# Kernel optimization log

Measured on AMD Instinct MI355X. Metric: run time of the kernel, lower is better.

## Reference

```python
import jax, jax.numpy as jnp
import numpy as np

G, DIN, DOUT, R = 8, 1024, 1024, 16
N = 8192
SCALE = 32.0 / 16.0  # alpha / r


def grouped_linear(x, W, mask):
    """Grouped linear: out[n] = x[n] @ W[g[n]].
    x: [N, din], W: [G, din, dout], mask: [N, G] one-hot (float).
    Computed as all-group matmul + select; the fused grouped-GEMM is the
    kernel opportunity this reference baselines."""
    y_all = jnp.einsum('ni,gio->gno', x, W)      # [G, N, dout]
    return jnp.einsum('gno,ng->no', y_all, mask)  # [N, dout]


def setup_inputs() -> dict:
    key = jax.random.key(0)
    k1, k2, k3, k4, k5 = jax.random.split(key, 5)
    x = jax.random.normal(k1, (N, DIN), dtype=jnp.float32)
    x_groups = jnp.sort(jax.random.randint(k2, (N,), 0, G, dtype=jnp.int64))
    W_base = jax.random.normal(k3, (G, DIN, DOUT), dtype=jnp.float32) * 0.02
    W_A = jax.random.normal(k4, (G, DIN, R), dtype=jnp.float32) * 0.02
    # original inits lora_B to zero; use small random values so the LoRA path
    # contributes nonzero signal for correctness testing
    W_B = jax.random.normal(k5, (G, R, DOUT), dtype=jnp.float32) * 0.02
    return {"x": x, "x_groups": x_groups, "W_base": W_base, "W_A": W_A, "W_B": W_B}


def reference(x, x_groups, W_base, W_A, W_B):
    mask = (x_groups[:, None] == jnp.arange(G)).astype(x.dtype)  # [N, G] one-hot
    base = grouped_linear(x, W_base, mask)            # base GroupedLinear
    a = grouped_linear(x, W_A, mask)                  # lora_A (dropout p=0 -> identity)
    adapt = grouped_linear(a, W_B, mask)              # lora_B
    return base + SCALE * adapt
```

## Files before the change

### kernel.cpp

```cpp
#include <hip/hip_runtime.h>
#include <stdint.h>

#define N_TOK 8192
#define DIN   1024
#define DOUT  1024
#define NG    8
#define LSCALE 2.0f

typedef __attribute__((ext_vector_type(4))) float  float4v;
typedef __attribute__((ext_vector_type(8))) short  short8;
typedef short8  frag_ab;
typedef float4v frag_cd;

__device__ __forceinline__ short f2bf(float f) {
    union { float f; uint32_t u; } v; v.f = f;
    uint32_t r = v.u + 0x7fffu + ((v.u >> 16) & 1u);
    return (short)(r >> 16);
}

__device__ __forceinline__ void load_lds16(const void* g, void* lds) {
    __builtin_amdgcn_global_load_lds(
        (const __attribute__((address_space(1))) uint32_t*)g,
        (__attribute__((address_space(3))) uint32_t*)lds,
        16, 0, 0);
}

#define PREP_GRID 6177

__global__ __launch_bounds__(256) void prep_kernel(
        const float* __restrict__ x, const float* __restrict__ Wb,
        const float* __restrict__ WA, const float* __restrict__ WB,
        const int* __restrict__ groups,
        short* __restrict__ xb, short* __restrict__ Wt,
        int* __restrict__ starts) {
    __shared__ float tile[64][65];
    __shared__ float Atr[16][72];
    __shared__ float Bt[16][64];
    const int blk = blockIdx.x, t = threadIdx.x;

    if (blk < 4096) {
        size_t idx = (size_t)(blk * 256 + t) * 8;
        const float4v* p = (const float4v*)(x + idx);
        float4v a = p[0], b = p[1];
        short8 o;
        o[0]=f2bf(a[0]); o[1]=f2bf(a[1]); o[2]=f2bf(a[2]); o[3]=f2bf(a[3]);
        o[4]=f2bf(b[0]); o[5]=f2bf(b[1]); o[6]=f2bf(b[2]); o[7]=f2bf(b[3]);
        *(short8*)(xb + idx) = o;
    } else if (blk < 6144) {
        int b = blk - 4096;
        int g = b >> 8, rem = b & 255;
        int n0 = (rem & 15) * 64, k0 = (rem >> 4) * 64;
        const float* Wg = Wb + (size_t)g * DIN * DOUT;
#pragma unroll
        for (int i = 0; i < 4; ++i) {
            int idx = i * 256 + t;
            int r = idx >> 4, c = (idx & 15) * 4;
            float4v v = *(const float4v*)(Wg + (size_t)(k0 + r) * DOUT + n0 + c);
            tile[r][c+0]=v[0]; tile[r][c+1]=v[1]; tile[r][c+2]=v[2]; tile[r][c+3]=v[3];
        }
        {
            int kk = t >> 2, c = (t & 3) * 4;
            float4v v = *(const float4v*)(WA + ((size_t)g * DIN + k0 + kk) * 16 + c);
            Atr[c+0][kk]=v[0]; Atr[c+1][kk]=v[1]; Atr[c+2][kk]=v[2]; Atr[c+3][kk]=v[3];
        }
        {
            int r = t >> 4, c = (t & 15) * 4;
            float4v v = *(const float4v*)(WB + ((size_t)g * 16 + r) * DOUT + n0 + c);
            Bt[r][c+0]=v[0]; Bt[r][c+1]=v[1]; Bt[r][c+2]=v[2]; Bt[r][c+3]=v[3];
        }
        __syncthreads();
        short* Wtg = Wt + (size_t)g * DOUT * DIN;
#pragma unroll
        for (int i = 0; i < 2; ++i) {
            int idx = i * 256 + t;
            int n = idx >> 3, c8 = (idx & 7) * 8;
            float corr[8] = {0.f,0.f,0.f,0.f,0.f,0.f,0.f,0.f};
#pragma unroll
            for (int r = 0; r < 16; ++r) {
                float bv = Bt[r][n];
                float4v a0 = *(const float4v*)&Atr[r][c8];
                float4v a1 = *(const float4v*)&Atr[r][c8 + 4];
                corr[0] += a0[0] * bv; corr[1] += a0[1] * bv;
                corr[2] += a0[2] * bv; corr[3] += a0[3] * bv;
                corr[4] += a1[0] * bv; corr[5] += a1[1] * bv;
                corr[6] += a1[2] * bv; corr[7] += a1[3] * bv;
            }
            short8 o;
#pragma unroll
            for (int j = 0; j < 8; ++j)
                o[j] = f2bf(tile[c8 + j][n] + LSCALE * corr[j]);
            *(short8*)(Wtg + (size_t)(n0 + n) * DIN + k0 + c8) = o;
        }
    } else {
        int i = (blk - 6144) * 256 + t;
        if (i > N_TOK) return;
        int cur  = (i < N_TOK) ? groups[i] : NG;
        int prev = (i == 0) ? -1 : groups[i - 1];
        for (int g = prev + 1; g <= cur; ++g) starts[g] = i;
    }
}

#define BM 128
#define BN 128
#define BK 64
#define NKT (DIN / BK)
#define MAXRT (N_TOK / BM + NG - 1)
#define GRID  (MAXRT * (DOUT / BN))

__global__ __launch_bounds__(256, 4)
void gemm_grouped(const short* __restrict__ xb,
                  const short* __restrict__ Wt,
                  const int*   __restrict__ starts,
                  float* __restrict__ out) {
    __shared__ short As[BM * BK];
    __shared__ short Bs[BN * BK];

    const int t    = threadIdx.x;
    const int lane = t & 63;
    const int wid  = t >> 6;
    const int L  = blockIdx.x;
    const int wg = (L & 7) * MAXRT + (L >> 3);
    const int rt = wg >> 3;
    const int ct = wg & 7;
    const int col0 = ct * BN;

    int g = -1, row0 = 0, rhi = 0;
    {
        int accum = 0;
#pragma unroll
        for (int gg = 0; gg < NG; ++gg) {
            int s0 = starts[gg], s1 = starts[gg + 1];
            int nt = (s1 - s0 + BM - 1) >> 7;
            if (g < 0 && rt < accum + nt) {
                g = gg;
                row0 = s0 + (rt - accum) * BM;
                rhi = (s1 < row0 + BM) ? s1 : row0 + BM;
            }
            accum += nt;
        }
    }
    if (g < 0) return;

    const short* wgp = Wt + (size_t)g * DOUT * DIN;
    const int wr  = (wid >> 1) * 64;
    const int wc  = (wid & 1) * 64;
    const int m16 = lane & 15;
    const int q   = lane >> 4;
    const int phase = ((L >> 3) & 3) * 4;

    frag_cd acc[4][4];
#pragma unroll
    for (int i = 0; i < 4; ++i)
#pragma unroll
        for (int j = 0; j < 4; ++j) { frag_cd z = {0.f,0.f,0.f,0.f}; acc[i][j] = z; }

    for (int kt_ii = 0; kt_ii < NKT; ++kt_ii) {
        const int kt = ((kt_ii + phase) & (NKT - 1)) * BK;

#pragma unroll
        for (int i = 0; i < 4; ++i) {
            int Lc = i * 256 + t;
            int r  = Lc >> 3;
            int c8 = (Lc & 7) ^ (r & 7);
            load_lds16(xb + (size_t)(row0 + r) * DIN + kt + c8 * 8,
                       &As[(i * 256 + wid * 64) * 8]);
        }
#pragma unroll
        for (int i = 0; i < 4; ++i) {
            int Lc = i * 256 + t;
            int r  = Lc >> 3;
            int c8 = (Lc & 7) ^ (r & 7);
            load_lds16(wgp + (size_t)(col0 + r) * DIN + kt + c8 * 8,
                       &Bs[(i * 256 + wid * 64) * 8]);
        }
        __syncthreads();

#pragma unroll
        for (int kk = 0; kk < BK; kk += 32) {
            frag_ab af[4], bf[4];
            const int ch = (kk >> 3) + q;
#pragma unroll
            for (int mi = 0; mi < 4; ++mi) {
                int rr = wr + mi * 16 + m16;
                af[mi] = *(const frag_ab*)&As[rr * BK + ((ch ^ (rr & 7)) << 3)];
            }
#pragma unroll
            for (int ni = 0; ni < 4; ++ni) {
                int cc = wc + ni * 16 + m16;
                bf[ni] = *(const frag_ab*)&Bs[cc * BK + ((ch ^ (cc & 7)) << 3)];
            }
#pragma unroll
            for (int mi = 0; mi < 4; ++mi)
#pragma unroll
                for (int ni = 0; ni < 4; ++ni)
                    acc[mi][ni] = __builtin_amdgcn_mfma_f32_16x16x32_bf16(
                        af[mi], bf[ni], acc[mi][ni], 0, 0, 0);
        }

        __syncthreads();
    }

#pragma unroll
    for (int mi = 0; mi < 4; ++mi)
#pragma unroll
        for (int r = 0; r < 4; ++r) {
            int grow = row0 + wr + mi * 16 + q * 4 + r;
            if (grow < rhi) {
                float* orow = out + (size_t)grow * DOUT + col0 + wc + m16;
#pragma unroll
                for (int ni = 0; ni < 4; ++ni)
                    __builtin_nontemporal_store(acc[mi][ni][r], orow + ni * 16);
            }
        }
}

extern "C" void kernel_launch(void* const* d_in, const int* in_sizes, int n_in,
                              void* d_out, int out_size, void* d_ws, size_t ws_size,
                              hipStream_t stream) {
    const float* x      = (const float*)d_in[0];
    const int*   groups = (const int*)d_in[1];
    const float* Wb     = (const float*)d_in[2];
    const float* WA     = (const float*)d_in[3];
    const float* WB     = (const float*)d_in[4];
    float* out = (float*)d_out;

    char* ws = (char*)d_ws;
    int*   starts = (int*)ws;
    short* xb     = (short*)(ws + 1024);
    short* Wt     = (short*)(ws + 1024 + (size_t)16 * 1024 * 1024);

    hipLaunchKernelGGL(prep_kernel, dim3(PREP_GRID), dim3(256), 0, stream,
                       x, Wb, WA, WB, groups, xb, Wt, starts);
    hipLaunchKernelGGL(gemm_grouped, dim3(GRID), dim3(256), 0, stream,
                       xb, Wt, starts, out);
}
```

Baseline: 139.1 us.

## Load B fragments directly from global into registers, drop B LDS tile

The weight (B) operand is no longer staged through shared memory. Each wave loads its B MFMA fragments straight from global memory into registers at the start of each k-tile, and the Bs LDS buffer and its fill loop are removed. Occupancy is lowered from 4 to 3 blocks per SM to make room for the extra registers. This aims to cut LDS traffic and footprint, at the cost of redundant global/L2 reads of B across the two waves sharing columns and less latency hiding, since the loads are issued just before use.

```diff
diff --git a/kernel.cpp b/kernel.cpp
--- a/kernel.cpp
+++ b/kernel.cpp
@@ -107,13 +107,12 @@
 #define MAXRT (N_TOK / BM + NG - 1)
 #define GRID  (MAXRT * (DOUT / BN))
 
-__global__ __launch_bounds__(256, 4)
+__global__ __launch_bounds__(256, 3)
 void gemm_grouped(const short* __restrict__ xb,
                   const short* __restrict__ Wt,
                   const int*   __restrict__ starts,
                   float* __restrict__ out) {
     __shared__ short As[BM * BK];
-    __shared__ short Bs[BN * BK];
 
     const int t    = threadIdx.x;
     const int lane = t & 63;
@@ -148,6 +147,11 @@
     const int q   = lane >> 4;
     const int phase = ((L >> 3) & 3) * 4;
 
+    const short* brow0 = wgp + (size_t)(col0 + wc +  0 + m16) * DIN + q * 8;
+    const short* brow1 = wgp + (size_t)(col0 + wc + 16 + m16) * DIN + q * 8;
+    const short* brow2 = wgp + (size_t)(col0 + wc + 32 + m16) * DIN + q * 8;
+    const short* brow3 = wgp + (size_t)(col0 + wc + 48 + m16) * DIN + q * 8;
+
     frag_cd acc[4][4];
 #pragma unroll
     for (int i = 0; i < 4; ++i)
@@ -156,6 +160,15 @@
 
     for (int kt_ii = 0; kt_ii < NKT; ++kt_ii) {
         const int kt = ((kt_ii + phase) & (NKT - 1)) * BK;
+
+        frag_ab b00 = *(const frag_ab*)(brow0 + kt);
+        frag_ab b01 = *(const frag_ab*)(brow1 + kt);
+        frag_ab b02 = *(const frag_ab*)(brow2 + kt);
+        frag_ab b03 = *(const frag_ab*)(brow3 + kt);
+        frag_ab b10 = *(const frag_ab*)(brow0 + kt + 32);
+        frag_ab b11 = *(const frag_ab*)(brow1 + kt + 32);
+        frag_ab b12 = *(const frag_ab*)(brow2 + kt + 32);
+        frag_ab b13 = *(const frag_ab*)(brow3 + kt + 32);
 
 #pragma unroll
         for (int i = 0; i < 4; ++i) {
@@ -165,36 +178,39 @@
             load_lds16(xb + (size_t)(row0 + r) * DIN + kt + c8 * 8,
                        &As[(i * 256 + wid * 64) * 8]);
         }
-#pragma unroll
-        for (int i = 0; i < 4; ++i) {
-            int Lc = i * 256 + t;
-            int r  = Lc >> 3;
-            int c8 = (Lc & 7) ^ (r & 7);
-            load_lds16(wgp + (size_t)(col0 + r) * DIN + kt + c8 * 8,
-                       &Bs[(i * 256 + wid * 64) * 8]);
-        }
         __syncthreads();
 
-#pragma unroll
-        for (int kk = 0; kk < BK; kk += 32) {
-            frag_ab af[4], bf[4];
-            const int ch = (kk >> 3) + q;
+        {
+            frag_ab af[4];
+            const int ch = q;
 #pragma unroll
             for (int mi = 0; mi < 4; ++mi) {
                 int rr = wr + mi * 16 + m16;
                 af[mi] = *(const frag_ab*)&As[rr * BK + ((ch ^ (rr & 7)) << 3)];
             }
 #pragma unroll
-            for (int ni = 0; ni < 4; ++ni) {
-                int cc = wc + ni * 16 + m16;
-                bf[ni] = *(const frag_ab*)&Bs[cc * BK + ((ch ^ (cc & 7)) << 3)];
-            }
-#pragma unroll
-            for (int mi = 0; mi < 4; ++mi)
-#pragma unroll
-                for (int ni = 0; ni < 4; ++ni)
-                    acc[mi][ni] = __builtin_amdgcn_mfma_f32_16x16x32_bf16(
-                        af[mi], bf[ni], acc[mi][ni], 0, 0, 0);
+            for (int mi = 0; mi < 4; ++mi) {
+                acc[mi][0] = __builtin_amdgcn_mfma_f32_16x16x32_bf16(af[mi], b00, acc[mi][0], 0, 0, 0);
+                acc[mi][1] = __builtin_amdgcn_mfma_f32_16x16x32_bf16(af[mi], b01, acc[mi][1], 0, 0, 0);
+                acc[mi][2] = __builtin_amdgcn_mfma_f32_16x16x32_bf16(af[mi], b02, acc[mi][2], 0, 0, 0);
+                acc[mi][3] = __builtin_amdgcn_mfma_f32_16x16x32_bf16(af[mi], b03, acc[mi][3], 0, 0, 0);
+            }
+        }
+        {
+            frag_ab af[4];
+            const int ch = 4 + q;
+#pragma unroll
+            for (int mi = 0; mi < 4; ++mi) {
+                int rr = wr + mi * 16 + m16;
+                af[mi] = *(const frag_ab*)&As[rr * BK + ((ch ^ (rr & 7)) << 3)];
+            }
+#pragma unroll
+            for (int mi = 0; mi < 4; ++mi) {
+                acc[mi][0] = __builtin_amdgcn_mfma_f32_16x16x32_bf16(af[mi], b10, acc[mi][0], 0, 0, 0);
+                acc[mi][1] = __builtin_amdgcn_mfma_f32_16x16x32_bf16(af[mi], b11, acc[mi][1], 0, 0, 0);
+                acc[mi][2] = __builtin_amdgcn_mfma_f32_16x16x32_bf16(af[mi], b12, acc[mi][2], 0, 0, 0);
+                acc[mi][3] = __builtin_amdgcn_mfma_f32_16x16x32_bf16(af[mi], b13, acc[mi][3], 0, 0, 0);
+            }
         }
 
         __syncthreads();
```

After: 168.5 us. 21.2% more time.
